# Optimization experiments

Measured on AMD Instinct MI355X. Metric: run time of the kernel, lower is better.

## Reference

```python
import jax, jax.numpy as jnp
import numpy as np

L, C, H, W = 16, 3, 512, 512
V_EPS = 1e-05


def setup_inputs() -> dict:
    key = jax.random.key(0)
    k1, k2, k3 = jax.random.split(key, 3)
    correct = jax.random.normal(k1, (L, C, H, W), dtype=jnp.float32)
    estimate = jax.random.normal(k2, (L, C, H, W), dtype=jnp.float32)
    mask = jax.random.uniform(k3, (L, C, H, W), dtype=jnp.float32)
    return {"correct": correct, "estimate": estimate, "mask": mask}


def reference(correct, estimate, mask):
    # Scale-invariant MSE, fully batched over (L, C) instead of Python loops.
    # v[l,c]   = sum_hw estimate^2 * mask
    # alpha    = sum_hw(correct*estimate*mask)/v  if v > 1e-5 else 0
    # err[l,c] = sum_hw mask * (correct - alpha*estimate)^2
    v = jnp.sum(estimate * estimate * mask, axis=(2, 3))              # [L, C]
    num = jnp.sum(correct * estimate * mask, axis=(2, 3))             # [L, C]
    cond = v > V_EPS
    alpha = jnp.where(cond, num / jnp.where(cond, v, 1.0), 0.0)       # [L, C]
    resid = correct - alpha[:, :, None, None] * estimate
    err = jnp.sum(mask * resid * resid, axis=(2, 3))                  # [L, C]
    masksum2 = jnp.sum(mask, axis=(2, 3))                             # [L, C]
    ssq = jnp.sum(err / masksum2, axis=1)                             # [L]
    return jnp.mean(ssq) / 3.0
```

## Files before the change

kernel.cpp:

```cpp
#include <hip/hip_runtime.h>

#define HW (512 * 512)
#define NCH 48
#define BPC 32
#define TPB 256
#define ITERS (HW / 4 / (BPC * TPB))
#define V_EPS 1e-5

__global__ __launch_bounds__(TPB) void smse_partials(
    const float* __restrict__ correct,
    const float* __restrict__ estimate,
    const float* __restrict__ mask,
    float4* __restrict__ partials)
{
    const int ch  = blockIdx.x / BPC;
    const int bin = blockIdx.x % BPC;

    const float4* __restrict__ c4 = (const float4*)(correct  + (size_t)ch * HW);
    const float4* __restrict__ e4 = (const float4*)(estimate + (size_t)ch * HW);
    const float4* __restrict__ m4 = (const float4*)(mask     + (size_t)ch * HW);

    const int stride = BPC * TPB;
    int i = bin * TPB + threadIdx.x;

    float se2m = 0.f, scem = 0.f, sc2m = 0.f, sm = 0.f;
    #pragma unroll
    for (int it = 0; it < ITERS; ++it, i += stride) {
        float4 c = c4[i];
        float4 e = e4[i];
        float4 m = m4[i];
        float em;
        em = e.x * m.x; se2m += e.x * em; scem += c.x * em; sc2m += c.x * c.x * m.x; sm += m.x;
        em = e.y * m.y; se2m += e.y * em; scem += c.y * em; sc2m += c.y * c.y * m.y; sm += m.y;
        em = e.z * m.z; se2m += e.z * em; scem += c.z * em; sc2m += c.z * c.z * m.z; sm += m.z;
        em = e.w * m.w; se2m += e.w * em; scem += c.w * em; sc2m += c.w * c.w * m.w; sm += m.w;
    }

    #pragma unroll
    for (int off = 32; off > 0; off >>= 1) {
        se2m += __shfl_down(se2m, off);
        scem += __shfl_down(scem, off);
        sc2m += __shfl_down(sc2m, off);
        sm   += __shfl_down(sm,   off);
    }

    __shared__ float4 red[TPB / 64];
    const int wave = threadIdx.x >> 6;
    const int lane = threadIdx.x & 63;
    if (lane == 0) red[wave] = make_float4(se2m, scem, sc2m, sm);
    __syncthreads();

    if (threadIdx.x == 0) {
        float4 s = red[0];
        #pragma unroll
        for (int w = 1; w < TPB / 64; ++w) {
            float4 r = red[w];
            s.x += r.x; s.y += r.y; s.z += r.z; s.w += r.w;
        }
        partials[(size_t)ch * BPC + bin] = s;
    }
}

__global__ __launch_bounds__(384) void smse_final(
    const float4* __restrict__ partials,
    float* __restrict__ out)
{
    const int t  = threadIdx.x;
    const int ch = t >> 3;
    const int k  = t & 7;

    const float4* p = partials + (size_t)ch * BPC + k * 4;
    float4 a = p[0], b = p[1], c = p[2], d = p[3];
    float sx = (a.x + b.x) + (c.x + d.x);
    float sy = (a.y + b.y) + (c.y + d.y);
    float sz = (a.z + b.z) + (c.z + d.z);
    float sw = (a.w + b.w) + (c.w + d.w);

    #pragma unroll
    for (int off = 4; off > 0; off >>= 1) {
        sx += __shfl_down(sx, off, 8);
        sy += __shfl_down(sy, off, 8);
        sz += __shfl_down(sz, off, 8);
        sw += __shfl_down(sw, off, 8);
    }

    __shared__ float chval[64];
    if (t < 64) chval[t] = 0.f;
    __syncthreads();
    if (k == 0) {
        double v = sx, num = sy, cc = sz, ms = sw;
        double alpha = (v > V_EPS) ? (num / v) : 0.0;
        double err = cc - alpha * (2.0 * num - alpha * v);
        chval[ch] = (float)(err / ms);
    }
    __syncthreads();

    if (t < 64) {
        float val = chval[t];
        #pragma unroll
        for (int off = 32; off > 0; off >>= 1) val += __shfl_down(val, off);
        if (t == 0) out[0] = val / (float)NCH;
    }
}

extern "C" void kernel_launch(void* const* d_in, const int* in_sizes, int n_in,
                              void* d_out, int out_size, void* d_ws, size_t ws_size,
                              hipStream_t stream) {
    const float* correct  = (const float*)d_in[0];
    const float* estimate = (const float*)d_in[1];
    const float* mask     = (const float*)d_in[2];
    float* out = (float*)d_out;
    float4* partials = (float4*)d_ws;

    smse_partials<<<NCH * BPC, TPB, 0, stream>>>(correct, estimate, mask, partials);
    smse_final<<<1, 384, 0, stream>>>(partials, out);
}
```

Before: 29.04 us.

## Split flat input evenly across blocks with channel-boundary lo/hi partials

Replaces per-channel block binning with a flat partition of all channels into 2048 contiguous chunks, each block accumulating separate sums for the two channels it may straddle. The final kernel maps block partials back to channels. This aims for better CU load balance and contiguous streaming per block, at the cost of extra accumulators, a per-iteration select, and a more complex final reduction.

```diff
diff --git a/kernel.cpp b/kernel.cpp
--- a/kernel.cpp
+++ b/kernel.cpp
@@ -2,62 +2,76 @@
 
 #define HW (512 * 512)
 #define NCH 48
-#define BPC 32
-#define TPB 256
-#define ITERS (HW / 4 / (BPC * TPB))
+#define CF4 (HW / 4)
+#define NF4 (NCH * CF4)
+#define GRID1 2048
+#define TPB1 256
+#define F4PB (NF4 / GRID1)
+#define IT1 (F4PB / TPB1)
 #define V_EPS 1e-5
 
-__global__ __launch_bounds__(TPB) void smse_partials(
+__global__ __launch_bounds__(TPB1) void smse_partials(
     const float* __restrict__ correct,
     const float* __restrict__ estimate,
     const float* __restrict__ mask,
     float4* __restrict__ partials)
 {
-    const int ch  = blockIdx.x / BPC;
-    const int bin = blockIdx.x % BPC;
+    const int b    = blockIdx.x;
+    const int base = b * F4PB;
+    const int chLo = base >> 16;
 
-    const float4* __restrict__ c4 = (const float4*)(correct  + (size_t)ch * HW);
-    const float4* __restrict__ e4 = (const float4*)(estimate + (size_t)ch * HW);
-    const float4* __restrict__ m4 = (const float4*)(mask     + (size_t)ch * HW);
+    const float4* __restrict__ c4 = (const float4*)correct;
+    const float4* __restrict__ e4 = (const float4*)estimate;
+    const float4* __restrict__ m4 = (const float4*)mask;
 
-    const int stride = BPC * TPB;
-    int i = bin * TPB + threadIdx.x;
+    float lo0 = 0.f, lo1 = 0.f, lo2 = 0.f, lo3 = 0.f;
+    float hi0 = 0.f, hi1 = 0.f, hi2 = 0.f, hi3 = 0.f;
 
-    float se2m = 0.f, scem = 0.f, sc2m = 0.f, sm = 0.f;
+    int i = base + threadIdx.x;
     #pragma unroll
-    for (int it = 0; it < ITERS; ++it, i += stride) {
+    for (int k = 0; k < IT1; ++k, i += TPB1) {
         float4 c = c4[i];
         float4 e = e4[i];
         float4 m = m4[i];
-        float em;
-        em = e.x * m.x; se2m += e.x * em; scem += c.x * em; sc2m += c.x * c.x * m.x; sm += m.x;
-        em = e.y * m.y; se2m += e.y * em; scem += c.y * em; sc2m += c.y * c.y * m.y; sm += m.y;
-        em = e.z * m.z; se2m += e.z * em; scem += c.z * em; sc2m += c.z * c.z * m.z; sm += m.z;
-        em = e.w * m.w; se2m += e.w * em; scem += c.w * em; sc2m += c.w * c.w * m.w; sm += m.w;
+        float s0 = 0.f, s1 = 0.f, s2 = 0.f, s3 = 0.f, em;
+        em = e.x * m.x; s0 += e.x * em; s1 += c.x * em; s2 += c.x * c.x * m.x; s3 += m.x;
+        em = e.y * m.y; s0 += e.y * em; s1 += c.y * em; s2 += c.y * c.y * m.y; s3 += m.y;
+        em = e.z * m.z; s0 += e.z * em; s1 += c.z * em; s2 += c.z * c.z * m.z; s3 += m.z;
+        em = e.w * m.w; s0 += e.w * em; s1 += c.w * em; s2 += c.w * c.w * m.w; s3 += m.w;
+        float fhi = ((i >> 16) != chLo) ? 1.f : 0.f;
+        float flo = 1.f - fhi;
+        lo0 += flo * s0; lo1 += flo * s1; lo2 += flo * s2; lo3 += flo * s3;
+        hi0 += fhi * s0; hi1 += fhi * s1; hi2 += fhi * s2; hi3 += fhi * s3;
     }
 
     #pragma unroll
     for (int off = 32; off > 0; off >>= 1) {
-        se2m += __shfl_down(se2m, off);
-        scem += __shfl_down(scem, off);
-        sc2m += __shfl_down(sc2m, off);
-        sm   += __shfl_down(sm,   off);
+        lo0 += __shfl_down(lo0, off); lo1 += __shfl_down(lo1, off);
+        lo2 += __shfl_down(lo2, off); lo3 += __shfl_down(lo3, off);
+        hi0 += __shfl_down(hi0, off); hi1 += __shfl_down(hi1, off);
+        hi2 += __shfl_down(hi2, off); hi3 += __shfl_down(hi3, off);
     }
 
-    __shared__ float4 red[TPB / 64];
+    __shared__ float4 redLo[TPB1 / 64];
+    __shared__ float4 redHi[TPB1 / 64];
     const int wave = threadIdx.x >> 6;
     const int lane = threadIdx.x & 63;
-    if (lane == 0) red[wave] = make_float4(se2m, scem, sc2m, sm);
+    if (lane == 0) {
+        redLo[wave] = make_float4(lo0, lo1, lo2, lo3);
+        redHi[wave] = make_float4(hi0, hi1, hi2, hi3);
+    }
     __syncthreads();
 
     if (threadIdx.x == 0) {
-        float4 s = red[0];
+        float4 slo = redLo[0], shi = redHi[0];
         #pragma unroll
-        for (int w = 1; w < TPB / 64; ++w) {
-            float4 r = red[w];
-            s.x += r.x; s.y += r.y; s.z += r.z; s.w += r.w;
+        for (int w = 1; w < TPB1 / 64; ++w) {
+            float4 a = redLo[w], b2 = redHi[w];
+            slo.x += a.x;  slo.y += a.y;  slo.z += a.z;  slo.w += a.w;
+            shi.x += b2.x; shi.y += b2.y; shi.z += b2.z; shi.w += b2.w;
         }
-        partials[(size_t)ch * BPC + bin] = s;
+        partials[2 * b]     = slo;
+        partials[2 * b + 1] = shi;
     }
 }
 
@@ -69,12 +83,22 @@
     const int ch = t >> 3;
     const int k  = t & 7;
 
-    const float4* p = partials + (size_t)ch * BPC + k * 4;
-    float4 a = p[0], b = p[1], c = p[2], d = p[3];
-    float sx = (a.x + b.x) + (c.x + d.x);
-    float sy = (a.y + b.y) + (c.y + d.y);
-    float sz = (a.z + b.z) + (c.z + d.z);
-    float sw = (a.w + b.w) + (c.w + d.w);
+    const int bstart = (ch * CF4) / F4PB;
+    const int bend   = ((ch + 1) * CF4 - 1) / F4PB;
+
+    float sx = 0.f, sy = 0.f, sz = 0.f, sw = 0.f;
+    #pragma unroll
+    for (int j = 0; j < 6; ++j) {
+        int b = bstart + k + 8 * j;
+        if (b <= bend) {
+            int cl = (b * F4PB) >> 16;
+            int chh = (b * F4PB + F4PB - 1) >> 16;
+            float4 lo = partials[2 * b];
+            float4 hi = partials[2 * b + 1];
+            if (cl == ch)  { sx += lo.x; sy += lo.y; sz += lo.z; sw += lo.w; }
+            if (chh == ch) { sx += hi.x; sy += hi.y; sz += hi.z; sw += hi.w; }
+        }
+    }
 
     #pragma unroll
     for (int off = 4; off > 0; off >>= 1) {
@@ -112,6 +136,6 @@
     float* out = (float*)d_out;
     float4* partials = (float4*)d_ws;
 
-    smse_partials<<<NCH * BPC, TPB, 0, stream>>>(correct, estimate, mask, partials);
+    smse_partials<<<GRID1, TPB1, 0, stream>>>(correct, estimate, mask, partials);
     smse_final<<<1, 384, 0, stream>>>(partials, out);
 }
```

New measurement: 31.81 us. 1.1x slower.
